# Kernel optimization log

Measured on AMD Instinct MI355X. Metric: run time of the kernel, lower is better.

## Reference

```python
import jax, jax.numpy as jnp
import numpy as np

N, E, G = 8192, 65536, 16          # atoms, edges, graphs in batch
NUM_ELEM, C, NB = 10, 64, 8        # elements, hidden channels, bessel basis
LMAX, NLAYERS = 3, 2
LM = (LMAX + 1) ** 2               # 16 spherical-harmonic components
R_MAX, P_CUT = 5.0, 5
EPS = 1e-9


def spherical_harmonics(u):
    # u: [E,3] unit vectors -> real spherical harmonics l<=3, [E,16]
    x, y, z = u[:, 0], u[:, 1], u[:, 2]
    x2, y2, z2 = x * x, y * y, z * z
    sh = [
        jnp.full_like(x, 0.28209479177387814),
        0.4886025119029199 * y, 0.4886025119029199 * z, 0.4886025119029199 * x,
        1.0925484305920792 * x * y, 1.0925484305920792 * y * z,
        0.31539156525252005 * (3.0 * z2 - 1.0),
        1.0925484305920792 * x * z, 0.5462742152960396 * (x2 - y2),
        0.5900435899266435 * y * (3.0 * x2 - y2), 2.890611442640554 * x * y * z,
        0.4570457994644658 * y * (5.0 * z2 - 1.0),
        0.3731763325901154 * z * (5.0 * z2 - 3.0),
        0.4570457994644658 * x * (5.0 * z2 - 1.0),
        1.445305721320277 * z * (x2 - y2),
        0.5900435899266435 * x * (x2 - 3.0 * y2),
    ]
    return jnp.stack(sh, axis=-1)


def radial_embedding(r):
    # Bessel radial basis with polynomial envelope cutoff -> [E, NB]
    u = r / R_MAX
    p = float(P_CUT)
    cut = (1.0 - 0.5 * (p + 1.0) * (p + 2.0) * u ** P_CUT
           + p * (p + 2.0) * u ** (P_CUT + 1)
           - 0.5 * p * (p + 1.0) * u ** (P_CUT + 2))
    cut = jnp.where(u < 1.0, cut, 0.0)
    n = jnp.arange(1, NB + 1, dtype=r.dtype)
    bessel = jnp.sqrt(2.0 / R_MAX) * jnp.sin(n[None, :] * jnp.pi * u[:, None]) \
             / jnp.maximum(r, EPS)[:, None]
    return bessel * cut[:, None]


def setup_inputs() -> dict:
    key = jax.random.key(0)
    ks = jax.random.split(key, 10)
    positions = jax.random.uniform(ks[0], (N, 3), jnp.float32) * 10.0
    elems = jax.random.randint(ks[1], (N,), 0, NUM_ELEM)
    node_attrs = jax.nn.one_hot(elems, NUM_ELEM, dtype=jnp.float32)
    edge_index = jax.random.randint(ks[2], (2, E), 0, N).astype(jnp.int32)
    shifts = jnp.zeros((E, 3), jnp.float32)
    batch = jnp.sort(jax.random.randint(ks[3], (N,), 0, G)).astype(jnp.int32)
    W_embed = jax.random.normal(ks[4], (NUM_ELEM, C), jnp.float32) / np.sqrt(NUM_ELEM)
    atomic_energies_w = jnp.arange(-1.0, -(NUM_ELEM + 1.0), -1.0, dtype=jnp.float32)
    W_rad = jax.random.normal(ks[5], (NLAYERS, NB, C), jnp.float32) / np.sqrt(NB)
    W_prod = jax.random.normal(ks[6], (NLAYERS, NUM_ELEM, (LMAX + 1) * C, C),
                               jnp.float32) / np.sqrt((LMAX + 1) * C)
    w_read = jax.random.normal(ks[7], (C,), jnp.float32) / np.sqrt(C)
    return {"positions": positions, "node_attrs": node_attrs, "shifts": shifts,
            "W_embed": W_embed, "atomic_energies_w": atomic_energies_w,
            "W_rad": W_rad, "W_prod": W_prod, "w_read": w_read,
            "edge_index": edge_index, "batch": batch}


def _energy(positions, node_attrs, shifts, W_embed, atomic_energies_w,
            W_rad, W_prod, w_read, edge_index, batch):
    snd, rcv = edge_index[0], edge_index[1]
    vec = positions[rcv] - positions[snd] + shifts            # [E,3]
    length = jnp.sqrt(jnp.sum(vec * vec, axis=-1) + EPS)      # [E]
    Y = spherical_harmonics(vec / length[:, None])            # [E,LM]
    R = radial_embedding(length)                              # [E,NB]

    e0 = jax.ops.segment_sum(node_attrs @ atomic_energies_w, batch, num_segments=G)
    h = node_attrs @ W_embed                                  # [N,C]

    for layer in range(NLAYERS):
        w = R @ W_rad[layer]                                  # [E,C] radial weights
        msg = (w * h[snd])[:, None, :] * Y[:, :, None]        # [E,LM,C] tensor product
        A = jax.ops.segment_sum(msg, rcv, num_segments=N)     # [N,LM,C] atomic basis
        A2 = A * A
        # invariant (rotation-invariant) contraction: sum over m within each l
        B = jnp.concatenate(
            [A2[:, l * l:(l + 1) * (l + 1), :].sum(axis=1) for l in range(LMAX + 1)],
            axis=-1)                                          # [N,(LMAX+1)*C]
        # element-dependent product-basis mixing
        h = jnp.einsum('nf,efc,ne->nc', B, W_prod[layer], node_attrs)

    node_e = h @ w_read                                       # [N]
    inter_e = jax.ops.segment_sum(node_e, batch, num_segments=G)
    return e0 + inter_e                                       # [G]


def reference(positions, node_attrs, shifts, W_embed, atomic_energies_w,
              W_rad, W_prod, w_read, edge_index, batch):
    energy = _energy(positions, node_attrs, shifts, W_embed, atomic_energies_w,
                     W_rad, W_prod, w_read, edge_index, batch)
    forces = -jax.grad(
        lambda p: _energy(p, node_attrs, shifts, W_embed, atomic_energies_w,
                          W_rad, W_prod, w_read, edge_index, batch).sum()
    )(positions)
    return energy, forces
```

## Files before the change

### kernel.cpp

```cpp
#include <hip/hip_runtime.h>
#include <math.h>

#define NN 8192
#define NE 65536
#define NG 16
#define NEL 10
#define CC 64
#define NLM 16
#define MAXST 32
#define PI_F 3.14159265358979f

__device__ __forceinline__ int lm_l(int lm) {
    return (lm == 0) ? 0 : (lm < 4) ? 1 : (lm < 9) ? 2 : 3;
}

__device__ __forceinline__ void stage_pack(
    const float* __restrict__ PK, const int* __restrict__ SSND,
    int beg, int cnt, int c, float* sPK, int* sS)
{
    int tot = cnt * 24;
    for (int i = c; i < tot; i += 64) sPK[i] = PK[(size_t)beg*24 + i];
    if (c < cnt) sS[c] = SSND[beg + c];
    __builtin_amdgcn_wave_barrier();
}

__global__ __launch_bounds__(256) void k_front(
    const float* __restrict__ pos, const float* __restrict__ shifts,
    const int* __restrict__ snd, const int* __restrict__ rcv,
    float* __restrict__ Y, float* __restrict__ R,
    float* __restrict__ U, float* __restrict__ L, int* __restrict__ cnt,
    const float* __restrict__ attrs, const float* __restrict__ Wemb,
    const float* __restrict__ aew, const int* __restrict__ batch,
    float* __restrict__ h0, int* __restrict__ elem, int* __restrict__ ecnt,
    float* __restrict__ out,
    const float* __restrict__ Wprod1, const float* __restrict__ wread,
    float* __restrict__ vb1)
{
    __shared__ int hcnt[NEL];
    int bx = blockIdx.x;
    if (bx < 256) {
        int e = bx * 256 + threadIdx.x;
        int s = snd[e], r = rcv[e];
        float vx = pos[r*3+0] - pos[s*3+0] + shifts[e*3+0];
        float vy = pos[r*3+1] - pos[s*3+1] + shifts[e*3+1];
        float vz = pos[r*3+2] - pos[s*3+2] + shifts[e*3+2];
        float len = sqrtf(vx*vx + vy*vy + vz*vz + 1e-9f);
        L[e] = len;
        if (len >= 5.0f) return;
        atomicAdd(&cnt[r], 1);
        float x = vx/len, y = vy/len, z = vz/len;
        U[e*3+0] = x; U[e*3+1] = y; U[e*3+2] = z;
        float x2 = x*x, y2 = y*y, z2 = z*z;
        float4* Yv = (float4*)(Y + (size_t)e*16);
        Yv[0] = make_float4(0.28209479177387814f,
                            0.4886025119029199f*y,
                            0.4886025119029199f*z,
                            0.4886025119029199f*x);
        Yv[1] = make_float4(1.0925484305920792f*x*y,
                            1.0925484305920792f*y*z,
                            0.31539156525252005f*(3.f*z2 - 1.f),
                            1.0925484305920792f*x*z);
        Yv[2] = make_float4(0.5462742152960396f*(x2 - y2),
                            0.5900435899266435f*y*(3.f*x2 - y2),
                            2.890611442640554f*x*y*z,
                            0.4570457994644658f*y*(5.f*z2 - 1.f));
        Yv[3] = make_float4(0.3731763325901154f*z*(5.f*z2 - 3.f),
                            0.4570457994644658f*x*(5.f*z2 - 1.f),
                            1.445305721320277f*z*(x2 - y2),
                            0.5900435899266435f*x*(x2 - 3.f*y2));
        float ur = len * 0.2f;
        float u2 = ur*ur, u4 = u2*u2, u5 = u4*ur, u6 = u5*ur, u7 = u6*ur;
        float cut = 1.f - 21.f*u5 + 35.f*u6 - 15.f*u7;
        const float s2f = 0.632455532033676f;
        float th = (PI_F/5.f) * len;
        float s1, c1; sincosf(th, &s1, &c1);
        float sn_ = s1, cs = c1;
        float coef = s2f * cut / len;
        float rv[8];
#pragma unroll
        for (int nb = 0; nb < 8; nb++) {
            rv[nb] = coef * sn_;
            float ns = sn_*c1 + cs*s1;
            float nc = cs*c1 - sn_*s1;
            sn_ = ns; cs = nc;
        }
        float4* Rv = (float4*)(R + (size_t)e*8);
        Rv[0] = make_float4(rv[0], rv[1], rv[2], rv[3]);
        Rv[1] = make_float4(rv[4], rv[5], rv[6], rv[7]);
    } else if (bx < 768) {
        int t = threadIdx.x, c = t & 63, w = t >> 6;
        if (t < NEL) hcnt[t] = 0;
        __syncthreads();
        float esum = 0.f; int curb = -1;
        for (int g = 0; g < 4; g++) {
            int n = (bx - 256)*16 + w*4 + g;
            float hv = 0.f;
            for (int el = 0; el < NEL; el++) hv += attrs[n*NEL+el] * Wemb[el*CC+c];
            h0[(size_t)n*CC+c] = hv;
            int el = 0; float e0 = 0.f;
            for (int k = 0; k < NEL; k++) {
                float a = attrs[n*NEL+k];
                e0 += a * aew[k];
                if (a > 0.5f) el = k;
            }
            if (c == 0) {
                elem[n] = el;
                atomicAdd(&hcnt[el], 1);
            }
            int b = batch[n];
            if (b != curb) {
                if (curb >= 0 && c == 0) atomicAdd(&out[curb], esum);
                curb = b; esum = 0.f;
            }
            esum += e0;
        }
        if (curb >= 0 && c == 0) atomicAdd(&out[curb], esum);
        __syncthreads();
        if (t < NEL) { int v = hcnt[t]; if (v) atomicAdd(&ecnt[t], v); }
    } else {
        int el = bx - 768, f = threadIdx.x;
        float s = 0.f;
        for (int c = 0; c < CC; c++) s += wread[c] * Wprod1[(size_t)el*256*CC + f*CC + c];
        vb1[el*256+f] = s;
    }
}

__global__ __launch_bounds__(1024) void k_scan(
    const int* __restrict__ cnt, int* __restrict__ offs,
    const int* __restrict__ ecnt, int* __restrict__ eoff)
{
    __shared__ int wsum[16];
    int t = threadIdx.x, lane = t & 63, w = t >> 6;
    int loc[8];
    int run = 0;
#pragma unroll
    for (int i = 0; i < 8; i++) { int v = cnt[t*8+i]; loc[i] = run; run += v; }
    int v = run;
#pragma unroll
    for (int o = 1; o < 64; o <<= 1) {
        int u = __shfl_up(v, o, 64);
        if (lane >= o) v += u;
    }
    if (lane == 63) wsum[w] = v;
    __syncthreads();
    if (t < 16) {
        int x = wsum[t];
#pragma unroll
        for (int o = 1; o < 16; o <<= 1) {
            int u = __shfl_up(x, o, 64);
            if (t >= o) x += u;
        }
        wsum[t] = x;
    }
    __syncthreads();
    int wpre = (w == 0) ? 0 : wsum[w-1];
    int pre = wpre + v - run;
#pragma unroll
    for (int i = 0; i < 8; i++) offs[t*8+i] = pre + loc[i];
    if (t == 1023) offs[NN] = pre + run;
    if (t == 0) {
        int r = 0;
        for (int el = 0; el < NEL; el++) { eoff[el] = r; r += ecnt[el]; }
        eoff[NEL] = r;
    }
}

__global__ void k_scatpack(
    const int* __restrict__ snd, const int* __restrict__ rcv,
    const float* __restrict__ Y, const float* __restrict__ R,
    const float* __restrict__ U, const float* __restrict__ L,
    const int* __restrict__ offs, int* __restrict__ cur,
    float* __restrict__ PK, int* __restrict__ SSND,
    float* __restrict__ UL,
    const int* __restrict__ elem, const int* __restrict__ eoff,
    int* __restrict__ ecur, int* __restrict__ nbe,
    float* __restrict__ gh1)
{
    int e = blockIdx.x * blockDim.x + threadIdx.x;
    {
        float4* g4 = (float4*)gh1;
        g4[e*2+0] = make_float4(0.f, 0.f, 0.f, 0.f);
        g4[e*2+1] = make_float4(0.f, 0.f, 0.f, 0.f);
    }
    if (e < NN) {
        int el = elem[e];
        int p = eoff[el] + atomicAdd(&ecur[el], 1);
        nbe[p] = e;
    }
    if (e >= NE) return;
    if (L[e] >= 5.0f) return;
    int r = rcv[e];
    int p = offs[r] + atomicAdd(&cur[r], 1);
    const float4* Yp = (const float4*)(Y + (size_t)e*16);
    float4* d = (float4*)(PK + (size_t)p*24);
    d[0] = Yp[0]; d[1] = Yp[1]; d[2] = Yp[2]; d[3] = Yp[3];
    const float4* Rp = (const float4*)(R + (size_t)e*8);
    d[4] = Rp[0]; d[5] = Rp[1];
    SSND[p] = snd[e];
    ((float4*)UL)[p] = make_float4(U[e*3+0], U[e*3+1], U[e*3+2], L[e]);
}

__global__ __launch_bounds__(256) void k_fwd0(
    const float* __restrict__ PK, const int* __restrict__ SSND,
    const float* __restrict__ Wrad0, const float* __restrict__ Wprod0,
    const float* __restrict__ h0, const float* __restrict__ attrs,
    const int* __restrict__ elem, const int* __restrict__ offs,
    const int* __restrict__ nbe, float* __restrict__ h1,
    float* __restrict__ A0)
{
    __shared__ __align__(16) float sB[4][1024];
    __shared__ __align__(16) float sPK[4][MAXST*24];
    __shared__ int sS[4][MAXST];
    int t = threadIdx.x, c = t & 63, w = t >> 6;
    float wr[8];
#pragma unroll
    for (int nb = 0; nb < 8; nb++) wr[nb] = Wrad0[nb*CC+c];
    int nid[4], nel[4]; float na[4];
#pragma unroll
    for (int g = 0; g < 4; g++) {
        int n = nbe[blockIdx.x*16 + w*4 + g];
        nid[g] = n;
        int el = elem[n]; nel[g] = el; na[g] = attrs[n*NEL+el];
        float acc[NLM];
#pragma unroll
        for (int lm = 0; lm < NLM; lm++) acc[lm] = 0.f;
        int beg = offs[n], end = offs[n+1];
        for (int base = beg; base < end; base += MAXST) {
            int m = min(MAXST, end - base);
            stage_pack(PK, SSND, base, m, c, sPK[w], sS[w]);
            for (int cb = 0; cb < m; cb += 4) {
                float hb[4];
#pragma unroll
                for (int k = 0; k < 4; k++)
                    hb[k] = (cb+k < m) ? h0[(size_t)sS[w][cb+k]*CC + c] : 0.f;
#pragma unroll
                for (int jj = 0; jj < 4; jj++) {
                    if (cb+jj >= m) break;
                    const float* rec = &sPK[w][(cb+jj)*24];
                    float wv = 0.f;
#pragma unroll
                    for (int nb = 0; nb < 8; nb++) wv += rec[16+nb]*wr[nb];
                    float tt = wv * hb[jj];
#pragma unroll
                    for (int lm = 0; lm < NLM; lm++) acc[lm] += rec[lm]*tt;
                }
            }
            __builtin_amdgcn_wave_barrier();
        }
#pragma unroll
        for (int lm = 0; lm < NLM; lm++) A0[(size_t)n*1024 + lm*64 + c] = acc[lm];
        float b0 = acc[0]*acc[0];
        float b1 = acc[1]*acc[1] + acc[2]*acc[2] + acc[3]*acc[3];
        float b2 = acc[4]*acc[4] + acc[5]*acc[5] + acc[6]*acc[6] + acc[7]*acc[7] + acc[8]*acc[8];
        float b3 = 0.f;
#pragma unroll
        for (int lm = 9; lm < 16; lm++) b3 += acc[lm]*acc[lm];
        sB[w][g*256 + 0*64 + c] = b0;
        sB[w][g*256 + 1*64 + c] = b1;
        sB[w][g*256 + 2*64 + c] = b2;
        sB[w][g*256 + 3*64 + c] = b3;
    }
    __builtin_amdgcn_wave_barrier();
    float hv[4] = {0.f, 0.f, 0.f, 0.f};
    int done = 0;
    while (done != 0xF) {
        int g0 = __ffs(~done & 0xF) - 1;
        int el = (g0==0) ? nel[0] : (g0==1) ? nel[1] : (g0==2) ? nel[2] : nel[3];
        int msk = 0;
#pragma unroll
        for (int g = 0; g < 4; g++) if (nel[g] == el) msk |= 1 << g;
        const float* Wn = Wprod0 + (size_t)el*256*CC;
        float tmp[4] = {0.f, 0.f, 0.f, 0.f};
        for (int f4 = 0; f4 < 64; f4++) {
            float wv0 = Wn[(f4*4+0)*CC + c];
            float wv1 = Wn[(f4*4+1)*CC + c];
            float wv2 = Wn[(f4*4+2)*CC + c];
            float wv3 = Wn[(f4*4+3)*CC + c];
#pragma unroll
            for (int g = 0; g < 4; g++) {
                float4 b = *((const float4*)&sB[w][g*256 + f4*4]);
                tmp[g] += b.x*wv0 + b.y*wv1 + b.z*wv2 + b.w*wv3;
            }
        }
#pragma unroll
        for (int g = 0; g < 4; g++) if ((msk >> g) & 1) hv[g] = tmp[g];
        done |= msk;
    }
#pragma unroll
    for (int g = 0; g < 4; g++) h1[(size_t)nid[g]*CC + c] = na[g]*hv[g];
}

__global__ __launch_bounds__(256) void k_fbwd1(
    const float* __restrict__ PK, const int* __restrict__ SSND,
    const float* __restrict__ Wrad1, const float* __restrict__ h1,
    const float* __restrict__ vb1,
    const float* __restrict__ attrs, const int* __restrict__ elem,
    const int* __restrict__ batch, const int* __restrict__ offs,
    float* __restrict__ gYp, float* __restrict__ gRp, float* __restrict__ gh,
    float* __restrict__ out)
{
    __shared__ __align__(16) float wrls[8*68];
    __shared__ __align__(16) float sPK[4][MAXST*24];
    __shared__ int sS[4][MAXST];
    __shared__ __align__(16) float Mls[4][16*68];
    __shared__ __align__(16) float Tls[4][4*68];
    __shared__ __align__(16) float Gls[4][4*68];
    int t = threadIdx.x, c = t & 63, w = t >> 6;
    float wr[8];
#pragma unroll
    for (int nb = 0; nb < 8; nb++) wr[nb] = Wrad1[nb*CC+c];
    if (w == 0) {
#pragma unroll
        for (int nb = 0; nb < 8; nb++) wrls[nb*68+c] = wr[nb];
    }
    __syncthreads();
    float esum = 0.f; int curb = -1;
    for (int g = 0; g < 4; g++) {
        int n = blockIdx.x*16 + w*4 + g;
        int el = elem[n];
        float a = attrs[n*NEL+el];
        float g4[4];
#pragma unroll
        for (int l = 0; l < 4; l++) g4[l] = a * vb1[el*256 + l*64 + c];
        int beg = offs[n], end = offs[n+1];
        int cnt = end - beg;
        float acc[NLM];
#pragma unroll
        for (int lm = 0; lm < NLM; lm++) acc[lm] = 0.f;
        for (int base = beg; base < end; base += MAXST) {
            int m = min(MAXST, end - base);
            stage_pack(PK, SSND, base, m, c, sPK[w], sS[w]);
            for (int cb = 0; cb < m; cb += 4) {
                float hb[4];
#pragma unroll
                for (int k = 0; k < 4; k++)
                    hb[k] = (cb+k < m) ? h1[(size_t)sS[w][cb+k]*CC + c] : 0.f;
#pragma unroll
                for (int jj = 0; jj < 4; jj++) {
                    if (cb+jj >= m) break;
                    const float* rec = &sPK[w][(cb+jj)*24];
                    float wv = 0.f;
#pragma unroll
                    for (int nb = 0; nb < 8; nb++) wv += rec[16+nb]*wr[nb];
                    float tt = wv * hb[jj];
#pragma unroll
                    for (int lm = 0; lm < NLM; lm++) acc[lm] += rec[lm]*tt;
                }
            }
            __builtin_amdgcn_wave_barrier();
        }
        bool cached = (cnt <= MAXST);
        float b0 = acc[0]*acc[0];
        float b1 = acc[1]*acc[1] + acc[2]*acc[2] + acc[3]*acc[3];
        float b2 = acc[4]*acc[4] + acc[5]*acc[5] + acc[6]*acc[6] + acc[7]*acc[7] + acc[8]*acc[8];
        float b3 = 0.f;
#pragma unroll
        for (int lm = 9; lm < 16; lm++) b3 += acc[lm]*acc[lm];
        float ep = b0*vb1[el*256+c] + b1*vb1[el*256+64+c]
                 + b2*vb1[el*256+128+c] + b3*vb1[el*256+192+c];
#pragma unroll
        for (int o = 32; o > 0; o >>= 1) ep += __shfl_xor(ep, o, 64);
        int b = batch[n];
        if (b != curb) {
            if (curb >= 0 && c == 0) atomicAdd(&out[curb], esum);
            curb = b; esum = 0.f;
        }
        esum += a * ep;
        float M[NLM];
#pragma unroll
        for (int lm = 0; lm < NLM; lm++) {
            M[lm] = 2.f * acc[lm] * g4[lm_l(lm)];
            Mls[w][lm*68+c] = M[lm];
        }
        __builtin_amdgcn_wave_barrier();
        for (int base = beg; base < end; base += MAXST) {
            int m = min(MAXST, end - base);
            if (!cached) stage_pack(PK, SSND, base, m, c, sPK[w], sS[w]);
            for (int cb = 0; cb < m; cb += 4) {
                int ncq = min(4, m - cb);
                float hb[4];
#pragma unroll
                for (int k = 0; k < 4; k++)
                    hb[k] = (cb+k < m) ? h1[(size_t)sS[w][cb+k]*CC + c] : 0.f;
#pragma unroll
                for (int jj = 0; jj < 4; jj++) {
                    if (jj >= ncq) break;
                    const float* rec = &sPK[w][(cb+jj)*24];
                    float wv = 0.f;
#pragma unroll
                    for (int nb = 0; nb < 8; nb++) wv += rec[16+nb]*wr[nb];
                    float hvv = hb[jj];
                    float my = 0.f;
#pragma unroll
                    for (int lm = 0; lm < NLM; lm++) my += M[lm]*rec[lm];
                    Tls[w][jj*68+c] = wv * hvv;
                    Gls[w][jj*68+c] = hvv * my;
                    atomicAdd(&gh[(size_t)sS[w][cb+jj]*CC + c], wv * my);
                }
                __builtin_amdgcn_wave_barrier();
                {
                    int jj = c >> 4, lm = c & 15;
                    if (jj < ncq) {
                        const float4* mrow = (const float4*)&Mls[w][lm*68];
                        const float4* trow = (const float4*)&Tls[w][jj*68];
                        float s_ = 0.f;
#pragma unroll
                        for (int k4 = 0; k4 < 16; k4++) {
                            float4 mm = mrow[k4]; float4 tv = trow[k4];
                            s_ += mm.x*tv.x + mm.y*tv.y + mm.z*tv.z + mm.w*tv.w;
                        }
                        gYp[(size_t)(base + cb + jj)*16+lm] = s_;
                    }
                }
                if (c < 32) {
                    int jj = c >> 3, nb = c & 7;
                    if (jj < ncq) {
                        const float4* wrow = (const float4*)&wrls[nb*68];
                        const float4* grow = (const float4*)&Gls[w][jj*68];
                        float s_ = 0.f;
#pragma unroll
                        for (int k4 = 0; k4 < 16; k4++) {
                            float4 wv4 = wrow[k4]; float4 gv = grow[k4];
                            s_ += wv4.x*gv.x + wv4.y*gv.y + wv4.z*gv.z + wv4.w*gv.w;
                        }
                        gRp[(size_t)(base + cb + jj)*8+nb] = s_;
                    }
                }
                __builtin_amdgcn_wave_barrier();
            }
        }
    }
    if (curb >= 0 && c == 0) atomicAdd(&out[curb], esum);
}

__global__ __launch_bounds__(256) void k_fbwd0geo(
    const float* __restrict__ PK, const int* __restrict__ SSND,
    const float* __restrict__ Wrad0, const float* __restrict__ h0,
    const float* __restrict__ gh1, const float* __restrict__ Wprod0,
    const float* __restrict__ A0,
    const float* __restrict__ attrs, const int* __restrict__ elem,
    const int* __restrict__ offs, const int* __restrict__ nbe,
    const float* __restrict__ gYp, const float* __restrict__ gRp,
    const float* __restrict__ UL, float* __restrict__ F)
{
    __shared__ __align__(16) float wrls[8*68];
    __shared__ __align__(16) float sPK[4][MAXST*24];
    __shared__ int sS[4][MAXST];
    __shared__ __align__(16) float Mls[4][16*68];
    __shared__ __align__(16) float Tls[4][4*68];
    __shared__ __align__(16) float Gls[4][4*68];
    __shared__ __align__(16) float sgh[4][4][64];
    __shared__ float gols[4][4*24];
    int t = threadIdx.x, c = t & 63, w = t >> 6;
    float wr[8];
#pragma unroll
    for (int nb = 0; nb < 8; nb++) wr[nb] = Wrad0[nb*CC+c];
    if (w == 0) {
#pragma unroll
        for (int nb = 0; nb < 8; nb++) wrls[nb*68+c] = wr[nb];
    }
    __syncthreads();
    int nid[4], nel[4]; float na[4];
#pragma unroll
    for (int g = 0; g < 4; g++) {
        int n = nbe[blockIdx.x*16 + w*4 + g];
        nid[g] = n;
        int el = elem[n]; nel[g] = el; na[g] = attrs[n*NEL+el];
        sgh[w][g][c] = gh1[(size_t)n*CC + c];
    }
    __builtin_amdgcn_wave_barrier();
    float outv[4][4];
    int done = 0;
    while (done != 0xF) {
        int g0 = __ffs(~done & 0xF) - 1;
        int el = (g0==0) ? nel[0] : (g0==1) ? nel[1] : (g0==2) ? nel[2] : nel[3];
        int msk = 0;
#pragma unroll
        for (int g = 0; g < 4; g++) if (nel[g] == el) msk |= 1 << g;
        const float* W0 = Wprod0 + (size_t)el*256*CC;
#pragma unroll
        for (int l = 0; l < 4; l++) {
            const float4* row = (const float4*)(W0 + (size_t)(l*64 + c)*CC);
            float t4[4] = {0.f, 0.f, 0.f, 0.f};
#pragma unroll 4
            for (int k4 = 0; k4 < 16; k4++) {
                float4 wv = row[k4];
#pragma unroll
                for (int g = 0; g < 4; g++) {
                    float4 gg = *((const float4*)&sgh[w][g][k4*4]);
                    t4[g] += wv.x*gg.x + wv.y*gg.y + wv.z*gg.z + wv.w*gg.w;
                }
            }
#pragma unroll
            for (int g = 0; g < 4; g++) if ((msk >> g) & 1) outv[l][g] = t4[g];
        }
        done |= msk;
    }
    for (int g = 0; g < 4; g++) {
        int n = nid[g];
        float g4[4];
#pragma unroll
        for (int l = 0; l < 4; l++) g4[l] = na[g]*outv[l][g];
        int beg = offs[n], end = offs[n+1];
        float acc[NLM];
#pragma unroll
        for (int lm = 0; lm < NLM; lm++) acc[lm] = A0[(size_t)n*1024 + lm*64 + c];
        float M[NLM];
#pragma unroll
        for (int lm = 0; lm < NLM; lm++) {
            M[lm] = 2.f * acc[lm] * g4[lm_l(lm)];
            Mls[w][lm*68+c] = M[lm];
        }
        __builtin_amdgcn_wave_barrier();
        for (int base = beg; base < end; base += MAXST) {
            int m = min(MAXST, end - base);
            stage_pack(PK, SSND, base, m, c, sPK[w], sS[w]);
            for (int cb = 0; cb < m; cb += 4) {
                int ncq = min(4, m - cb);
                float hb[4];
#pragma unroll
                for (int k = 0; k < 4; k++)
                    hb[k] = (cb+k < m) ? h0[(size_t)sS[w][cb+k]*CC + c] : 0.f;
#pragma unroll
                for (int jj = 0; jj < 4; jj++) {
                    if (jj >= ncq) break;
                    const float* rec = &sPK[w][(cb+jj)*24];
                    float wv = 0.f;
#pragma unroll
                    for (int nb = 0; nb < 8; nb++) wv += rec[16+nb]*wr[nb];
                    float hvv = hb[jj];
                    float my = 0.f;
#pragma unroll
                    for (int lm = 0; lm < NLM; lm++) my += M[lm]*rec[lm];
                    Tls[w][jj*68+c] = wv * hvv;
                    Gls[w][jj*68+c] = hvv * my;
                }
                __builtin_amdgcn_wave_barrier();
                {
                    int jj = c >> 4, lm = c & 15;
                    if (jj < ncq) {
                        const float4* mrow = (const float4*)&Mls[w][lm*68];
                        const float4* trow = (const float4*)&Tls[w][jj*68];
                        float s_ = 0.f;
#pragma unroll
                        for (int k4 = 0; k4 < 16; k4++) {
                            float4 mm = mrow[k4]; float4 tv = trow[k4];
                            s_ += mm.x*tv.x + mm.y*tv.y + mm.z*tv.z + mm.w*tv.w;
                        }
                        gols[w][jj*24+lm] = s_ + gYp[(size_t)(base + cb + jj)*16+lm];
                    }
                }
                if (c < 32) {
                    int jj = c >> 3, nb = c & 7;
                    if (jj < ncq) {
                        const float4* wrow = (const float4*)&wrls[nb*68];
                        const float4* grow = (const float4*)&Gls[w][jj*68];
                        float s_ = 0.f;
#pragma unroll
                        for (int k4 = 0; k4 < 16; k4++) {
                            float4 wv4 = wrow[k4]; float4 gv = grow[k4];
                            s_ += wv4.x*gv.x + wv4.y*gv.y + wv4.z*gv.z + wv4.w*gv.w;
                        }
                        gols[w][jj*24+16+nb] = s_ + gRp[(size_t)(base + cb + jj)*8+nb];
                    }
                }
                __builtin_amdgcn_wave_barrier();
                if ((c & 15) == 0) {
                    int jj = c >> 4;
                    if (jj < ncq) {
                        int pp = base + cb + jj;
                        const float* go = &gols[w][jj*24];
                        float4 ul = ((const float4*)UL)[pp];
                        float x = ul.x, y = ul.y, z = ul.z, len = ul.w;
                        float x2 = x*x, y2 = y*y, z2 = z*z;
                        float gx = 0.f, gy = 0.f, gz = 0.f;
                        gx += 0.4886025119029199f*go[3];
                        gy += 0.4886025119029199f*go[1];
                        gz += 0.4886025119029199f*go[2];
                        gx += 1.0925484305920792f*y*go[4];  gy += 1.0925484305920792f*x*go[4];
                        gy += 1.0925484305920792f*z*go[5];  gz += 1.0925484305920792f*y*go[5];
                        gz += 1.8923493915151203f*z*go[6];
                        gx += 1.0925484305920792f*z*go[7];  gz += 1.0925484305920792f*x*go[7];
                        gx += 1.0925484305920792f*x*go[8];  gy -= 1.0925484305920792f*y*go[8];
                        gx += 3.540261539559861f*x*y*go[9];
                        gy += 0.5900435899266435f*(3.f*x2 - 3.f*y2)*go[9];
                        gx += 2.890611442640554f*y*z*go[10]; gy += 2.890611442640554f*x*z*go[10]; gz += 2.890611442640554f*x*y*go[10];
                        gy += 0.4570457994644658f*(5.f*z2 - 1.f)*go[11]; gz += 4.570457994644658f*y*z*go[11];
                        gz += 0.3731763325901154f*(15.f*z2 - 3.f)*go[12];
                        gx += 0.4570457994644658f*(5.f*z2 - 1.f)*go[13]; gz += 4.570457994644658f*x*z*go[13];
                        gx += 2.890611442640554f*x*z*go[14]; gy -= 2.890611442640554f*y*z*go[14];
                        gz += 1.445305721320277f*(x2 - y2)*go[14];
                        gx += 0.5900435899266435f*(3.f*x2 - 3.f*y2)*go[15];
                        gy -= 3.540261539559861f*x*y*go[15];
                        float ur = len * 0.2f;
                        float u2 = ur*ur, u4 = u2*u2, u5 = u4*ur, u6 = u5*ur, u7 = u6*ur;
                        float poly  = 1.f - 21.f*u5 + 35.f*u6 - 15.f*u7;
                        float dpoly = (-105.f*u4 + 210.f*u5 - 105.f*u6)*0.2f;
                        const float s2f = 0.632455532033676f;
                        const float k1 = PI_F/5.f;
                        float th = k1*len;
                        float s1, c1; sincosf(th, &s1, &c1);
                        float sn_ = s1, cs = c1;
                        float inv_r = 1.f/len;
                        bool tiny = (len < 2e-3f);
                        float gL = 0.f;
#pragma unroll
                        for (int nb = 0; nb < 8; nb++) {
                            float kn = k1*(float)(nb+1);
                            float bes = s2f*sn_*inv_r;
                            float dbes;
                            if (tiny) dbes = -s2f*kn*kn*kn*len*(1.f/3.f);
                            else      dbes = s2f*(kn*cs - sn_*inv_r)*inv_r;
                            gL += go[16+nb]*(dbes*poly + bes*dpoly);
                            float ns = sn_*c1 + cs*s1;
                            float nc = cs*c1 - sn_*s1;
                            sn_ = ns; cs = nc;
                        }
                        float dot = gx*x + gy*y + gz*z;
                        float gvx = (gx - dot*x)*inv_r + gL*x;
                        float gvy = (gy - dot*y)*inv_r + gL*y;
                        float gvz = (gz - dot*z)*inv_r + gL*z;
                        int sn2 = sS[w][cb+jj];
                        atomicAdd(&F[n*3+0], -gvx);
                        atomicAdd(&F[n*3+1], -gvy);
                        atomicAdd(&F[n*3+2], -gvz);
                        atomicAdd(&F[sn2*3+0],  gvx);
                        atomicAdd(&F[sn2*3+1],  gvy);
                        atomicAdd(&F[sn2*3+2],  gvz);
                    }
                }
                __builtin_amdgcn_wave_barrier();
            }
        }
    }
}

extern "C" void kernel_launch(void* const* d_in, const int* in_sizes, int n_in,
                              void* d_out, int out_size, void* d_ws, size_t ws_size,
                              hipStream_t stream)
{
    const float* positions  = (const float*)d_in[0];
    const float* node_attrs = (const float*)d_in[1];
    const float* shifts     = (const float*)d_in[2];
    const float* W_embed    = (const float*)d_in[3];
    const float* aew        = (const float*)d_in[4];
    const float* W_rad      = (const float*)d_in[5];
    const float* W_prod     = (const float*)d_in[6];
    const float* w_read     = (const float*)d_in[7];
    const int*   edge_index = (const int*)d_in[8];
    const int*   batch      = (const int*)d_in[9];
    float* out = (float*)d_out;

    const int* snd = edge_index;
    const int* rcv = edge_index + NE;

    char* ws = (char*)d_ws;
    size_t off = 0;
    auto allocf = [&](size_t nelems) -> float* {
        float* p = (float*)(ws + off); off += nelems * sizeof(float); return p;
    };
    float* Y    = allocf((size_t)NE*16);
    float* R    = allocf((size_t)NE*8);
    float* U    = allocf((size_t)NE*3);
    float* L    = allocf((size_t)NE);
    float* PK   = allocf((size_t)NE*24);
    float* UL   = allocf((size_t)NE*4);
    float* H0   = allocf((size_t)NN*CC);
    float* H1   = allocf((size_t)NN*CC);
    float* A0   = allocf((size_t)NN*1024);
    float* GYP  = allocf((size_t)NE*16);
    float* GRP  = allocf((size_t)NE*8);
    float* VB1  = allocf((size_t)NEL*256);
    float* GH1  = allocf((size_t)NN*CC);
    size_t zero_off = off;
    int* CNT   = (int*)(ws + off); off += (size_t)NN*4;
    int* CUR   = (int*)(ws + off); off += (size_t)NN*4;
    int* ECNT  = (int*)(ws + off); off += 16*4;
    int* ECUR  = (int*)(ws + off); off += 16*4;
    size_t zero_bytes = off - zero_off;
    int* ELEM  = (int*)(ws + off); off += (size_t)NN*4;
    int* OFFS  = (int*)(ws + off); off += (size_t)(NN+1)*4;
    int* SSND  = (int*)(ws + off); off += (size_t)NE*4;
    int* ELOFF = (int*)(ws + off); off += 16*4;
    int* NBE   = (int*)(ws + off); off += (size_t)NN*4;

    hipMemsetAsync(out, 0, (size_t)out_size * sizeof(float), stream);
    hipMemsetAsync(ws + zero_off, 0, zero_bytes, stream);

    const float* Wrad0  = W_rad;
    const float* Wrad1  = W_rad + 8*CC;
    const float* Wprod0 = W_prod;
    const float* Wprod1 = W_prod + (size_t)NEL*256*CC;

    k_front<<<256 + 512 + NEL, 256, 0, stream>>>(
        positions, shifts, snd, rcv, Y, R, U, L, CNT,
        node_attrs, W_embed, aew, batch, H0, ELEM, ECNT, out,
        Wprod1, w_read, VB1);
    k_scan<<<1, 1024, 0, stream>>>(CNT, OFFS, ECNT, ELOFF);
    k_scatpack<<<NE/256, 256, 0, stream>>>(snd, rcv, Y, R, U, L, OFFS, CUR,
                                           PK, SSND, UL, ELEM, ELOFF, ECUR, NBE, GH1);

    k_fwd0<<<NN/16, 256, 0, stream>>>(PK, SSND, Wrad0, Wprod0, H0, node_attrs, ELEM,
                                      OFFS, NBE, H1, A0);
    k_fbwd1<<<NN/16, 256, 0, stream>>>(PK, SSND, Wrad1, H1, VB1, node_attrs, ELEM,
                                       batch, OFFS, GYP, GRP, GH1, out);
    k_fbwd0geo<<<NN/16, 256, 0, stream>>>(PK, SSND, Wrad0, H0, GH1, Wprod0, A0,
                                          node_attrs, ELEM, OFFS, NBE,
                                          GYP, GRP, UL, out + NG);
    (void)in_sizes; (void)n_in; (void)ws_size;
}
```

Before: 271.7 us.

## Register-prefetch next edge chunk while processing current one in gather kernels

Splits the LDS staging of packed edge records into a register load and an LDS store, and prefetches the next chunk (possibly belonging to the next node in the wave's group) into registers while the current chunk is being processed. The goal is to hide global-memory latency of the PK/SSND stage behind the per-edge accumulation in k_fwd0, the layer-1 kernel, and the layer-0 backward kernel. It costs 13 extra live registers per thread, which may reduce occupancy, and adds chunk-advance bookkeeping across nodes.

```diff
diff --git a/kernel.cpp b/kernel.cpp
--- a/kernel.cpp
+++ b/kernel.cpp
@@ -14,14 +14,42 @@
     return (lm == 0) ? 0 : (lm < 4) ? 1 : (lm < 9) ? 2 : 3;
 }
 
-__device__ __forceinline__ void stage_pack(
+struct Pref { float v[12]; int s; };
+
+__device__ __forceinline__ void stage_load(
     const float* __restrict__ PK, const int* __restrict__ SSND,
-    int beg, int cnt, int c, float* sPK, int* sS)
-{
-    int tot = cnt * 24;
-    for (int i = c; i < tot; i += 64) sPK[i] = PK[(size_t)beg*24 + i];
-    if (c < cnt) sS[c] = SSND[beg + c];
+    int beg, int m, int c, Pref& r)
+{
+    int tot = m * 24;
+    const float* src = PK + (size_t)beg * 24;
+#pragma unroll
+    for (int k = 0; k < 12; k++) {
+        int i = c + k*64;
+        r.v[k] = (i < tot) ? src[i] : 0.f;
+    }
+    r.s = (c < m) ? SSND[beg + c] : 0;
+}
+
+__device__ __forceinline__ void stage_store(const Pref& r, int m, int c,
+                                            float* sPK, int* sS)
+{
+    int tot = m * 24;
+#pragma unroll
+    for (int k = 0; k < 12; k++) {
+        int i = c + k*64;
+        if (i < tot) sPK[i] = r.v[k];
+    }
+    if (c < m) sS[c] = r.s;
     __builtin_amdgcn_wave_barrier();
+}
+
+__device__ __forceinline__ void stage_sync(
+    const float* __restrict__ PK, const int* __restrict__ SSND,
+    int beg, int m, int c, float* sPK, int* sS)
+{
+    Pref r;
+    stage_load(PK, SSND, beg, m, c, r);
+    stage_store(r, m, c, sPK, sS);
 }
 
 __global__ __launch_bounds__(256) void k_front(
@@ -200,6 +228,11 @@
     ((float4*)UL)[p] = make_float4(U[e*3+0], U[e*3+1], U[e*3+2], L[e]);
 }
 
+#define ADV_CHUNK()                                                      \
+    do { cbase += MAXST;                                                 \
+         while (cg < 4 && cbase >= ends[cg]) { cg++; if (cg < 4) cbase = begs[cg]; } \
+    } while (0)
+
 __global__ __launch_bounds__(256) void k_fwd0(
     const float* __restrict__ PK, const int* __restrict__ SSND,
     const float* __restrict__ Wrad0, const float* __restrict__ Wprod0,
@@ -216,18 +249,28 @@
 #pragma unroll
     for (int nb = 0; nb < 8; nb++) wr[nb] = Wrad0[nb*CC+c];
     int nid[4], nel[4]; float na[4];
+    int begs[4], ends[4];
 #pragma unroll
     for (int g = 0; g < 4; g++) {
         int n = nbe[blockIdx.x*16 + w*4 + g];
         nid[g] = n;
         int el = elem[n]; nel[g] = el; na[g] = attrs[n*NEL+el];
+        begs[g] = offs[n]; ends[g] = offs[n+1];
+    }
+    int cg = 0, cbase = begs[0];
+    while (cg < 4 && cbase >= ends[cg]) { cg++; if (cg < 4) cbase = begs[cg]; }
+    Pref pre;
+    if (cg < 4) stage_load(PK, SSND, cbase, min(MAXST, ends[cg]-cbase), c, pre);
+
+    for (int g = 0; g < 4; g++) {
         float acc[NLM];
 #pragma unroll
         for (int lm = 0; lm < NLM; lm++) acc[lm] = 0.f;
-        int beg = offs[n], end = offs[n+1];
-        for (int base = beg; base < end; base += MAXST) {
-            int m = min(MAXST, end - base);
-            stage_pack(PK, SSND, base, m, c, sPK[w], sS[w]);
+        for (int base = begs[g]; base < ends[g]; base += MAXST) {
+            int m = min(MAXST, ends[g] - base);
+            stage_store(pre, m, c, sPK[w], sS[w]);
+            ADV_CHUNK();
+            if (cg < 4) stage_load(PK, SSND, cbase, min(MAXST, ends[cg]-cbase), c, pre);
             for (int cb = 0; cb < m; cb += 4) {
                 float hb[4];
 #pragma unroll
@@ -248,7 +291,7 @@
             __builtin_amdgcn_wave_barrier();
         }
 #pragma unroll
-        for (int lm = 0; lm < NLM; lm++) A0[(size_t)n*1024 + lm*64 + c] = acc[lm];
+        for (int lm = 0; lm < NLM; lm++) A0[(size_t)nid[g]*1024 + lm*64 + c] = acc[lm];
         float b0 = acc[0]*acc[0];
         float b1 = acc[1]*acc[1] + acc[2]*acc[2] + acc[3]*acc[3];
         float b2 = acc[4]*acc[4] + acc[5]*acc[5] + acc[6]*acc[6] + acc[7]*acc[7] + acc[8]*acc[8];
@@ -314,6 +357,17 @@
         for (int nb = 0; nb < 8; nb++) wrls[nb*68+c] = wr[nb];
     }
     __syncthreads();
+    int begs[4], ends[4];
+#pragma unroll
+    for (int g = 0; g < 4; g++) {
+        int n = blockIdx.x*16 + w*4 + g;
+        begs[g] = offs[n]; ends[g] = offs[n+1];
+    }
+    int cg = 0, cbase = begs[0];
+    while (cg < 4 && cbase >= ends[cg]) { cg++; if (cg < 4) cbase = begs[cg]; }
+    Pref pre;
+    if (cg < 4) stage_load(PK, SSND, cbase, min(MAXST, ends[cg]-cbase), c, pre);
+
     float esum = 0.f; int curb = -1;
     for (int g = 0; g < 4; g++) {
         int n = blockIdx.x*16 + w*4 + g;
@@ -322,14 +376,16 @@
         float g4[4];
 #pragma unroll
         for (int l = 0; l < 4; l++) g4[l] = a * vb1[el*256 + l*64 + c];
-        int beg = offs[n], end = offs[n+1];
+        int beg = begs[g], end = ends[g];
         int cnt = end - beg;
         float acc[NLM];
 #pragma unroll
         for (int lm = 0; lm < NLM; lm++) acc[lm] = 0.f;
         for (int base = beg; base < end; base += MAXST) {
             int m = min(MAXST, end - base);
-            stage_pack(PK, SSND, base, m, c, sPK[w], sS[w]);
+            stage_store(pre, m, c, sPK[w], sS[w]);
+            ADV_CHUNK();
+            if (cg < 4) stage_load(PK, SSND, cbase, min(MAXST, ends[cg]-cbase), c, pre);
             for (int cb = 0; cb < m; cb += 4) {
                 float hb[4];
 #pragma unroll
@@ -375,7 +431,7 @@
         __builtin_amdgcn_wave_barrier();
         for (int base = beg; base < end; base += MAXST) {
             int m = min(MAXST, end - base);
-            if (!cached) stage_pack(PK, SSND, base, m, c, sPK[w], sS[w]);
+            if (!cached) stage_sync(PK, SSND, base, m, c, sPK[w], sS[w]);
             for (int cb = 0; cb < m; cb += 4) {
                 int ncq = min(4, m - cb);
                 float hb[4];
@@ -461,14 +517,20 @@
     }
     __syncthreads();
     int nid[4], nel[4]; float na[4];
+    int begs[4], ends[4];
 #pragma unroll
     for (int g = 0; g < 4; g++) {
         int n = nbe[blockIdx.x*16 + w*4 + g];
         nid[g] = n;
         int el = elem[n]; nel[g] = el; na[g] = attrs[n*NEL+el];
+        begs[g] = offs[n]; ends[g] = offs[n+1];
         sgh[w][g][c] = gh1[(size_t)n*CC + c];
     }
     __builtin_amdgcn_wave_barrier();
+    int cg = 0, cbase = begs[0];
+    while (cg < 4 && cbase >= ends[cg]) { cg++; if (cg < 4) cbase = begs[cg]; }
+    Pref pre;
+    if (cg < 4) stage_load(PK, SSND, cbase, min(MAXST, ends[cg]-cbase), c, pre);
     float outv[4][4];
     int done = 0;
     while (done != 0xF) {
@@ -501,7 +563,7 @@
         float g4[4];
 #pragma unroll
         for (int l = 0; l < 4; l++) g4[l] = na[g]*outv[l][g];
-        int beg = offs[n], end = offs[n+1];
+        int beg = begs[g], end = ends[g];
         float acc[NLM];
 #pragma unroll
         for (int lm = 0; lm < NLM; lm++) acc[lm] = A0[(size_t)n*1024 + lm*64 + c];
@@ -514,7 +576,9 @@
         __builtin_amdgcn_wave_barrier();
         for (int base = beg; base < end; base += MAXST) {
             int m = min(MAXST, end - base);
-            stage_pack(PK, SSND, base, m, c, sPK[w], sS[w]);
+            stage_store(pre, m, c, sPK[w], sS[w]);
+            ADV_CHUNK();
+            if (cg < 4) stage_load(PK, SSND, cbase, min(MAXST, ends[cg]-cbase), c, pre);
             for (int cb = 0; cb < m; cb += 4) {
                 int ncq = min(4, m - cb);
                 float hb[4];
```

Result: no change. 272.9 us (+0.5%).

## Sort atoms by degree and element to balance per-wave work in node kernels

Applied to the files above, without the earlier changes.

Node ordering (nbe) is now built by bucketing atoms on capped in-degree (descending) and element, using a histogram computed inside the scan kernel, instead of by element alone. k_fbwd1 also iterates nodes through this permutation, so the waves of a block handle atoms with similar neighbour counts, which reduces load imbalance and divergence in the per-edge loops. The e0/readout energy accumulation moves into k_fbwd1 as a per-node atomic, and the output memset is folded into k_scatpack. The cost is more global atomics on the energy output and a less sequential memory access order.

```diff
diff --git a/kernel.cpp b/kernel.cpp
--- a/kernel.cpp
+++ b/kernel.cpp
@@ -8,6 +8,7 @@
 #define CC 64
 #define NLM 16
 #define MAXST 32
+#define NBKT 160
 #define PI_F 3.14159265358979f
 
 __device__ __forceinline__ int lm_l(int lm) {
@@ -30,13 +31,10 @@
     float* __restrict__ Y, float* __restrict__ R,
     float* __restrict__ U, float* __restrict__ L, int* __restrict__ cnt,
     const float* __restrict__ attrs, const float* __restrict__ Wemb,
-    const float* __restrict__ aew, const int* __restrict__ batch,
-    float* __restrict__ h0, int* __restrict__ elem, int* __restrict__ ecnt,
-    float* __restrict__ out,
+    float* __restrict__ h0, int* __restrict__ elem,
     const float* __restrict__ Wprod1, const float* __restrict__ wread,
     float* __restrict__ vb1)
 {
-    __shared__ int hcnt[NEL];
     int bx = blockIdx.x;
     if (bx < 256) {
         int e = bx * 256 + threadIdx.x;
@@ -89,34 +87,18 @@
         Rv[1] = make_float4(rv[4], rv[5], rv[6], rv[7]);
     } else if (bx < 768) {
         int t = threadIdx.x, c = t & 63, w = t >> 6;
-        if (t < NEL) hcnt[t] = 0;
-        __syncthreads();
-        float esum = 0.f; int curb = -1;
         for (int g = 0; g < 4; g++) {
             int n = (bx - 256)*16 + w*4 + g;
             float hv = 0.f;
             for (int el = 0; el < NEL; el++) hv += attrs[n*NEL+el] * Wemb[el*CC+c];
             h0[(size_t)n*CC+c] = hv;
-            int el = 0; float e0 = 0.f;
-            for (int k = 0; k < NEL; k++) {
-                float a = attrs[n*NEL+k];
-                e0 += a * aew[k];
-                if (a > 0.5f) el = k;
+            if (c == 0) {
+                int el = 0;
+                for (int k = 0; k < NEL; k++)
+                    if (attrs[n*NEL+k] > 0.5f) el = k;
+                elem[n] = el;
             }
-            if (c == 0) {
-                elem[n] = el;
-                atomicAdd(&hcnt[el], 1);
-            }
-            int b = batch[n];
-            if (b != curb) {
-                if (curb >= 0 && c == 0) atomicAdd(&out[curb], esum);
-                curb = b; esum = 0.f;
-            }
-            esum += e0;
-        }
-        if (curb >= 0 && c == 0) atomicAdd(&out[curb], esum);
-        __syncthreads();
-        if (t < NEL) { int v = hcnt[t]; if (v) atomicAdd(&ecnt[t], v); }
+        }
     } else {
         int el = bx - 768, f = threadIdx.x;
         float s = 0.f;
@@ -127,14 +109,17 @@
 
 __global__ __launch_bounds__(1024) void k_scan(
     const int* __restrict__ cnt, int* __restrict__ offs,
-    const int* __restrict__ ecnt, int* __restrict__ eoff)
+    const int* __restrict__ elem, int* __restrict__ boff)
 {
     __shared__ int wsum[16];
+    __shared__ int hist[NBKT];
     int t = threadIdx.x, lane = t & 63, w = t >> 6;
-    int loc[8];
+    if (t < NBKT) hist[t] = 0;
+    __syncthreads();
+    int cv[8], loc[8];
     int run = 0;
 #pragma unroll
-    for (int i = 0; i < 8; i++) { int v = cnt[t*8+i]; loc[i] = run; run += v; }
+    for (int i = 0; i < 8; i++) { int v = cnt[t*8+i]; cv[i] = v; loc[i] = run; run += v; }
     int v = run;
 #pragma unroll
     for (int o = 1; o < 64; o <<= 1) {
@@ -158,10 +143,16 @@
 #pragma unroll
     for (int i = 0; i < 8; i++) offs[t*8+i] = pre + loc[i];
     if (t == 1023) offs[NN] = pre + run;
+#pragma unroll
+    for (int i = 0; i < 8; i++) {
+        int n = t*8+i;
+        int key = (15 - min(cv[i], 15))*NEL + elem[n];
+        atomicAdd(&hist[key], 1);
+    }
+    __syncthreads();
     if (t == 0) {
         int r = 0;
-        for (int el = 0; el < NEL; el++) { eoff[el] = r; r += ecnt[el]; }
-        eoff[NEL] = r;
+        for (int k = 0; k < NBKT; k++) { boff[k] = r; r += hist[k]; }
     }
 }
 
@@ -172,9 +163,9 @@
     const int* __restrict__ offs, int* __restrict__ cur,
     float* __restrict__ PK, int* __restrict__ SSND,
     float* __restrict__ UL,
-    const int* __restrict__ elem, const int* __restrict__ eoff,
-    int* __restrict__ ecur, int* __restrict__ nbe,
-    float* __restrict__ gh1)
+    const int* __restrict__ elem, const int* __restrict__ boff,
+    int* __restrict__ bcur, int* __restrict__ nbe,
+    float* __restrict__ gh1, float* __restrict__ out)
 {
     int e = blockIdx.x * blockDim.x + threadIdx.x;
     {
@@ -182,9 +173,11 @@
         g4[e*2+0] = make_float4(0.f, 0.f, 0.f, 0.f);
         g4[e*2+1] = make_float4(0.f, 0.f, 0.f, 0.f);
     }
+    if (e < NG + NN*3) out[e] = 0.f;
     if (e < NN) {
-        int el = elem[e];
-        int p = eoff[el] + atomicAdd(&ecur[el], 1);
+        int deg = offs[e+1] - offs[e];
+        int key = (15 - min(deg, 15))*NEL + elem[e];
+        int p = boff[key] + atomicAdd(&bcur[key], 1);
         nbe[p] = e;
     }
     if (e >= NE) return;
@@ -248,7 +241,7 @@
             __builtin_amdgcn_wave_barrier();
         }
 #pragma unroll
-        for (int lm = 0; lm < NLM; lm++) A0[(size_t)n*1024 + lm*64 + c] = acc[lm];
+        for (int lm = 0; lm < NLM; lm++) A0[(size_t)nid[g]*1024 + lm*64 + c] = acc[lm];
         float b0 = acc[0]*acc[0];
         float b1 = acc[1]*acc[1] + acc[2]*acc[2] + acc[3]*acc[3];
         float b2 = acc[4]*acc[4] + acc[5]*acc[5] + acc[6]*acc[6] + acc[7]*acc[7] + acc[8]*acc[8];
@@ -294,8 +287,10 @@
     const float* __restrict__ PK, const int* __restrict__ SSND,
     const float* __restrict__ Wrad1, const float* __restrict__ h1,
     const float* __restrict__ vb1,
-    const float* __restrict__ attrs, const int* __restrict__ elem,
+    const float* __restrict__ attrs, const float* __restrict__ aew,
+    const int* __restrict__ elem,
     const int* __restrict__ batch, const int* __restrict__ offs,
+    const int* __restrict__ nbe,
     float* __restrict__ gYp, float* __restrict__ gRp, float* __restrict__ gh,
     float* __restrict__ out)
 {
@@ -314,9 +309,8 @@
         for (int nb = 0; nb < 8; nb++) wrls[nb*68+c] = wr[nb];
     }
     __syncthreads();
-    float esum = 0.f; int curb = -1;
     for (int g = 0; g < 4; g++) {
-        int n = blockIdx.x*16 + w*4 + g;
+        int n = nbe[blockIdx.x*16 + w*4 + g];
         int el = elem[n];
         float a = attrs[n*NEL+el];
         float g4[4];
@@ -360,12 +354,11 @@
                  + b2*vb1[el*256+128+c] + b3*vb1[el*256+192+c];
 #pragma unroll
         for (int o = 32; o > 0; o >>= 1) ep += __shfl_xor(ep, o, 64);
-        int b = batch[n];
-        if (b != curb) {
-            if (curb >= 0 && c == 0) atomicAdd(&out[curb], esum);
-            curb = b; esum = 0.f;
-        }
-        esum += a * ep;
+        if (c == 0) {
+            float e0 = 0.f;
+            for (int k = 0; k < NEL; k++) e0 += attrs[n*NEL+k] * aew[k];
+            atomicAdd(&out[batch[n]], a*ep + e0);
+        }
         float M[NLM];
 #pragma unroll
         for (int lm = 0; lm < NLM; lm++) {
@@ -430,7 +423,6 @@
             }
         }
     }
-    if (curb >= 0 && c == 0) atomicAdd(&out[curb], esum);
 }
 
 __global__ __launch_bounds__(256) void k_fbwd0geo(
@@ -675,16 +667,14 @@
     size_t zero_off = off;
     int* CNT   = (int*)(ws + off); off += (size_t)NN*4;
     int* CUR   = (int*)(ws + off); off += (size_t)NN*4;
-    int* ECNT  = (int*)(ws + off); off += 16*4;
-    int* ECUR  = (int*)(ws + off); off += 16*4;
+    int* BCUR  = (int*)(ws + off); off += NBKT*4;
     size_t zero_bytes = off - zero_off;
     int* ELEM  = (int*)(ws + off); off += (size_t)NN*4;
     int* OFFS  = (int*)(ws + off); off += (size_t)(NN+1)*4;
     int* SSND  = (int*)(ws + off); off += (size_t)NE*4;
-    int* ELOFF = (int*)(ws + off); off += 16*4;
+    int* BOFF  = (int*)(ws + off); off += NBKT*4;
     int* NBE   = (int*)(ws + off); off += (size_t)NN*4;
 
-    hipMemsetAsync(out, 0, (size_t)out_size * sizeof(float), stream);
     hipMemsetAsync(ws + zero_off, 0, zero_bytes, stream);
 
     const float* Wrad0  = W_rad;
@@ -694,18 +684,18 @@
 
     k_front<<<256 + 512 + NEL, 256, 0, stream>>>(
         positions, shifts, snd, rcv, Y, R, U, L, CNT,
-        node_attrs, W_embed, aew, batch, H0, ELEM, ECNT, out,
-        Wprod1, w_read, VB1);
-    k_scan<<<1, 1024, 0, stream>>>(CNT, OFFS, ECNT, ELOFF);
+        node_attrs, W_embed, H0, ELEM, Wprod1, w_read, VB1);
+    k_scan<<<1, 1024, 0, stream>>>(CNT, OFFS, ELEM, BOFF);
     k_scatpack<<<NE/256, 256, 0, stream>>>(snd, rcv, Y, R, U, L, OFFS, CUR,
-                                           PK, SSND, UL, ELEM, ELOFF, ECUR, NBE, GH1);
+                                           PK, SSND, UL, ELEM, BOFF, BCUR, NBE,
+                                           GH1, out);
 
     k_fwd0<<<NN/16, 256, 0, stream>>>(PK, SSND, Wrad0, Wprod0, H0, node_attrs, ELEM,
                                       OFFS, NBE, H1, A0);
-    k_fbwd1<<<NN/16, 256, 0, stream>>>(PK, SSND, Wrad1, H1, VB1, node_attrs, ELEM,
-                                       batch, OFFS, GYP, GRP, GH1, out);
+    k_fbwd1<<<NN/16, 256, 0, stream>>>(PK, SSND, Wrad1, H1, VB1, node_attrs, aew, ELEM,
+                                       batch, OFFS, NBE, GYP, GRP, GH1, out);
     k_fbwd0geo<<<NN/16, 256, 0, stream>>>(PK, SSND, Wrad0, H0, GH1, Wprod0, A0,
                                           node_attrs, ELEM, OFFS, NBE,
                                           GYP, GRP, UL, out + NG);
-    (void)in_sizes; (void)n_in; (void)ws_size;
-}
+    (void)in_sizes; (void)n_in; (void)out_size; (void)ws_size;
+}
```

Result: slower. 365.6 us (+34.6%).
